# Kernel optimization log

Hardware: AMD Instinct MI355X
Metric: run time of the kernel (lower is better)

Reference implementation:

```python
import jax, jax.numpy as jnp
import numpy as np

N, F, H, C = 2048, 32, 64, 2
NEG = 0.01  # leaky_relu slope
BN_EPS = 1e-5


def _bn(h, g, b):
    m = h.mean(axis=0)
    v = h.var(axis=0)  # biased, as torch BN uses for normalization
    return (h - m) * jax.lax.rsqrt(v + BN_EPS) * g + b


def _gin(x, src, dst, eps, Wa, ba, Wb, bb):
    # PyG GINConv: out = mlp((1+eps)*x + sum_{j->i} x_j), messages flow src->dst
    agg = jax.ops.segment_sum(x[src], dst, num_segments=N)
    h = (1.0 + eps) * x + agg
    h = jax.nn.relu(h @ Wa + ba)
    return jax.nn.relu(h @ Wb + bb)


def setup_inputs() -> dict:
    key = jax.random.key(0)
    ks = jax.random.split(key, 16)
    src_np, dst_np = np.triu_indices(N, k=1)  # torch.combinations(arange(N), r=2)
    d = {
        'x': jnp.zeros((1,), jnp.float32),
        'node_features': jax.random.uniform(ks[0], (N, F), jnp.float32),
        'eps1': jnp.zeros((), jnp.float32),
        'W1a': jax.random.normal(ks[1], (F, H), jnp.float32) * 0.1,
        'b1a': jnp.zeros((H,), jnp.float32),
        'W1b': jax.random.normal(ks[2], (H, H), jnp.float32) * 0.1,
        'b1b': jnp.zeros((H,), jnp.float32),
        'epsm': jnp.zeros((), jnp.float32),
        'Wma': jax.random.normal(ks[3], (H, H), jnp.float32) * 0.1,
        'bma': jnp.zeros((H,), jnp.float32),
        'Wmb': jax.random.normal(ks[4], (H, H), jnp.float32) * 0.1,
        'bmb': jnp.zeros((H,), jnp.float32),
        'bnm_g': jnp.ones((H,), jnp.float32),
        'bnm_b': jnp.zeros((H,), jnp.float32),
        'epsl': jnp.zeros((), jnp.float32),
        'Wla': jax.random.normal(ks[5], (H, H), jnp.float32) * 0.1,
        'bla': jnp.zeros((H,), jnp.float32),
        'Wlb': jax.random.normal(ks[6], (H, F), jnp.float32) * 0.1,
        'blb': jnp.zeros((F,), jnp.float32),
        'W5': jax.random.normal(ks[7], (F, H), jnp.float32) * 0.1,
        'b5': jnp.zeros((H,), jnp.float32),
        'bn5_g': jnp.ones((H,), jnp.float32),
        'bn5_b': jnp.zeros((H,), jnp.float32),
        'W6': jax.random.normal(ks[8], (H, C), jnp.float32) * 0.1,
        'b6': jnp.zeros((C,), jnp.float32),
        'edge_src': jnp.asarray(src_np, jnp.int32),
        'edge_dst': jnp.asarray(dst_np, jnp.int32),
    }
    return d


def reference(x, node_features, eps1, W1a, b1a, W1b, b1b,
              epsm, Wma, bma, Wmb, bmb, bnm_g, bnm_b,
              epsl, Wla, bla, Wlb, blb,
              W5, b5, bn5_g, bn5_b, W6, b6,
              edge_src, edge_dst):
    xinit = node_features
    h = node_features
    # conv1 + leaky_relu
    h = jax.nn.leaky_relu(_gin(h, edge_src, edge_dst, eps1, W1a, b1a, W1b, b1b), NEG)
    # middle conv + leaky_relu + BN
    h = _gin(h, edge_src, edge_dst, epsm, Wma, bma, Wmb, bmb)
    h = jax.nn.leaky_relu(h, NEG)
    h = _bn(h, bnm_g, bnm_b)
    # last conv (back to F channels)
    h = _gin(h, edge_src, edge_dst, epsl, Wla, bla, Wlb, blb)
    h = h + xinit
    # edge predictor: gather-mul-MLP
    x_i = h[edge_src]
    x_j = h[edge_dst]
    e = jax.nn.leaky_relu((x_i * x_j) @ W5 + b5, NEG)
    e = _bn(e, bn5_g, bn5_b)
    logits = e @ W6 + b6
    p = jax.nn.softmax(logits, axis=-1)  # [E, C]
    # scatter into symmetric dense NxNxC tensor
    probs = jnp.zeros((N, N, C), jnp.float32)
    probs = probs.at[edge_src, edge_dst].set(p)
    probs = probs.at[edge_dst, edge_src].set(p)
    return probs
```

## Files before the change

kernel.cpp:

```cpp
#include <hip/hip_runtime.h>
#include <math.h>

#define NN 2048

typedef __attribute__((ext_vector_type(8))) short short8;
typedef __attribute__((ext_vector_type(4))) float f32x4;

__device__ inline short f2bf(float x) {
  union { float f; unsigned u; } v; v.f = x;
  unsigned r = v.u + 0x7fff + ((v.u >> 16) & 1);
  return (short)(r >> 16);
}
__device__ inline float bf2f(short h) {
  union { unsigned u; float f; } t;
  t.u = ((unsigned)(unsigned short)h) << 16;
  return t.f;
}

__global__ __launch_bounds__(256) void k_init(
    const float* __restrict__ nf, const float* __restrict__ W5,
    float* __restrict__ cs1, short* __restrict__ w5hi, short* __restrict__ w5lo,
    double* __restrict__ zbase) {
  __shared__ float sm[256];
  int tid = threadIdx.x, blk = blockIdx.x;
  int gtid = blk * 256 + tid;
  int node0 = blk * 32;
  if (gtid < 10240) zbase[gtid] = 0.0;
  if (gtid < 2048) {
    int c = gtid >> 5, k = gtid & 31;
    float wv = W5[k * 64 + c];
    short hi = f2bf(wv);
    w5hi[c * 32 + k] = hi;
    w5lo[c * 32 + k] = f2bf(wv - bf2f(hi));
  }
  int f = tid & 31, g = tid >> 5;
  float acc = 0.f;
#pragma unroll
  for (int k = 0; k < 4; k++) acc += nf[(size_t)(node0 + g * 4 + k) * 32 + f];
  sm[g * 32 + f] = acc;
  __syncthreads();
  if (tid < 32) {
    float s = 0.f;
#pragma unroll
    for (int g2 = 0; g2 < 8; g2++) s += sm[g2 * 32 + tid];
    cs1[blk * 32 + tid] = s;
  }
}

template <int FIN, int FOUT, bool STATS, bool ADDX, bool AFFINE, bool CSUM>
__global__ __launch_bounds__(256) void k_mlp32(
    const float* __restrict__ X, const float* __restrict__ CS,
    const float* __restrict__ epsp,
    const float* __restrict__ Wa, const float* __restrict__ ba,
    const float* __restrict__ Wb, const float* __restrict__ bb,
    float* __restrict__ OUT, const float* __restrict__ XINIT,
    double* __restrict__ statsW, const double* __restrict__ statsRd,
    const float* __restrict__ bng, const float* __restrict__ bnb,
    float* __restrict__ csum) {
  __shared__ float xh[32 * (FIN + 1)];
  __shared__ float Ts[32 * 65];
  __shared__ float Was[FIN * 64];
  __shared__ float Wbs[64 * FOUT];
  __shared__ float spref[FIN];
  __shared__ float part[4 * FIN];
  __shared__ float bas[64];
  __shared__ float bbs[FOUT];
  __shared__ float ssum[64];
  __shared__ float ssq[64];
  __shared__ float affa[64];
  __shared__ float affb[64];
  int tid = threadIdx.x;
  int blk = blockIdx.x;
  int node0 = blk * 32;
  float ep = 1.f + epsp[0];

  if (AFFINE) {
    if (tid < 64) {
      double s1 = 0.0, s2 = 0.0;
#pragma unroll
      for (int r = 0; r < 16; r++) {
        s1 += statsRd[r * 128 + tid];
        s2 += statsRd[r * 128 + 64 + tid];
      }
      double mean = s1 * (1.0 / 2048.0);
      double var = s2 * (1.0 / 2048.0) - mean * mean;
      if (var < 0.0) var = 0.0;
      float a = (float)((double)bng[tid] / sqrt(var + 1e-5));
      affa[tid] = a;
      affb[tid] = fmaf(-(float)mean, a, bnb[tid]);
    }
    __syncthreads();
  }

  for (int idx = tid; idx < 32 * FIN / 4; idx += 256) {
    int row = idx / (FIN / 4), c4 = (idx % (FIN / 4)) * 4;
    float4 v = *(const float4*)(X + (size_t)(node0 + row) * FIN + c4);
    if (AFFINE) {
      v.x = fmaf(affa[c4 + 0], v.x, affb[c4 + 0]);
      v.y = fmaf(affa[c4 + 1], v.y, affb[c4 + 1]);
      v.z = fmaf(affa[c4 + 2], v.z, affb[c4 + 2]);
      v.w = fmaf(affa[c4 + 3], v.w, affb[c4 + 3]);
    }
    float* dst = xh + row * (FIN + 1) + c4;
    dst[0] = v.x; dst[1] = v.y; dst[2] = v.z; dst[3] = v.w;
  }
  if (tid < 4 * FIN) {
    int g = tid / FIN, f = tid % FIN;
    float s = 0.f;
    for (int c = g; c < blk; c += 4) s += CS[c * FIN + f];
    part[tid] = s;
  }
  for (int idx = tid; idx < FIN * 16; idx += 256)
    *(float4*)(Was + idx * 4) = *(const float4*)(Wa + idx * 4);
  for (int idx = tid; idx < FOUT * 16; idx += 256)
    *(float4*)(Wbs + idx * 4) = *(const float4*)(Wb + idx * 4);
  if (tid < 64) bas[tid] = ba[tid];
  if (tid < FOUT) bbs[tid] = bb[tid];
  if ((STATS || CSUM) && tid < 64) { ssum[tid] = 0.f; ssq[tid] = 0.f; }
  __syncthreads();

  if (tid < FIN) {
    float s = part[tid] + part[FIN + tid] + part[2 * FIN + tid] + part[3 * FIN + tid];
    if (AFFINE) s = fmaf(affa[tid], s, (float)(32 * blk) * affb[tid]);
    spref[tid] = s;
  }
  __syncthreads();

  {
    int w = tid >> 6, lane = tid & 63, half = lane >> 5, nl = lane & 31;
#pragma unroll
    for (int p = 0; p < FIN / 8; p++) {
      int f = w * (FIN / 4) + 2 * p + half;
      float v = xh[nl * (FIN + 1) + f];
      float s = v;
#pragma unroll
      for (int d = 1; d < 32; d <<= 1) {
        float t = __shfl_up(s, (unsigned)d, 32);
        if (nl >= d) s += t;
      }
      xh[nl * (FIN + 1) + f] = fmaf(ep, v, spref[f] + (s - v));
    }
  }
  __syncthreads();

  {
    int n = tid >> 3, c0 = (tid & 7) * 8;
    float acc[8];
#pragma unroll
    for (int k = 0; k < 8; k++) acc[k] = bas[c0 + k];
    for (int f = 0; f < FIN; f++) {
      float xv = xh[n * (FIN + 1) + f];
#pragma unroll
      for (int k = 0; k < 8; k++) acc[k] = fmaf(xv, Was[f * 64 + c0 + k], acc[k]);
    }
#pragma unroll
    for (int k = 0; k < 8; k++) Ts[n * 65 + c0 + k] = fmaxf(acc[k], 0.f);
  }
  __syncthreads();

  {
    constexpr int CC = FOUT / 8;
    int n = tid >> 3, c0 = (tid & 7) * CC;
    float acc[CC];
#pragma unroll
    for (int k = 0; k < CC; k++) acc[k] = bbs[c0 + k];
    for (int f = 0; f < 64; f++) {
      float tv = Ts[n * 65 + f];
#pragma unroll
      for (int k = 0; k < CC; k++) acc[k] = fmaf(tv, Wbs[f * FOUT + c0 + k], acc[k]);
    }
#pragma unroll
    for (int k = 0; k < CC; k++) {
      float r = fmaxf(acc[k], 0.f);
      if (STATS || CSUM) atomicAdd(&ssum[c0 + k], r);
      if (STATS) atomicAdd(&ssq[c0 + k], r * r);
      if (ADDX) r += XINIT[(size_t)(node0 + n) * FOUT + c0 + k];
      OUT[(size_t)(node0 + n) * FOUT + c0 + k] = r;
    }
  }
  if (STATS || CSUM) {
    __syncthreads();
    if (tid < FOUT) {
      if (CSUM) csum[blk * FOUT + tid] = ssum[tid];
      if (STATS) {
        int rep = blk & 15;
        atomicAdd(&statsW[rep * 128 + tid], (double)ssum[tid]);
        atomicAdd(&statsW[rep * 128 + 64 + tid], (double)ssq[tid]);
      }
    }
  }
}

__device__ inline void tile_decode(int t, int& bi, int& bj) {
  bi = (int)((257.0f - sqrtf(66049.0f - 8.0f * (float)t)) * 0.5f);
  if (bi > 127) bi = 127;
  while (bi > 0 && bi * (257 - bi) / 2 > t) bi--;
  while ((bi + 1) * (256 - bi) / 2 <= t) bi++;
  bj = bi + (t - bi * (257 - bi) / 2);
}

__device__ inline void split_pack(const float m[8], short8& ah, short8& al) {
  unsigned uh[8], ul[8];
#pragma unroll
  for (int e = 0; e < 8; e++) {
    union { float f; unsigned u; } um; um.f = m[e];
    uh[e] = um.u;
    union { unsigned u; float f; } hf; hf.u = um.u & 0xffff0000u;
    union { float f; unsigned u; } lf; lf.f = m[e] - hf.f;
    ul[e] = lf.u;
  }
  union { unsigned i[4]; short8 s; } ph, pl;
#pragma unroll
  for (int k = 0; k < 4; k++) {
    ph.i[k] = __builtin_amdgcn_perm(uh[2 * k + 1], uh[2 * k], 0x07060302u);
    pl.i[k] = __builtin_amdgcn_perm(ul[2 * k + 1], ul[2 * k], 0x07060302u);
  }
  ah = ph.s;
  al = pl.s;
}

__device__ inline f32x4 mfma3b(short8 ah, short8 al, short8 bh, short8 bl, float bias) {
  f32x4 z = (f32x4){bias, bias, bias, bias};
  z = __builtin_amdgcn_mfma_f32_16x16x32_bf16(al, bh, z, 0, 0, 0);
  z = __builtin_amdgcn_mfma_f32_16x16x32_bf16(ah, bl, z, 0, 0, 0);
  z = __builtin_amdgcn_mfma_f32_16x16x32_bf16(ah, bh, z, 0, 0, 0);
  return z;
}

__global__ __launch_bounds__(256) void k_edge1m(
    const float* __restrict__ H3, const short* __restrict__ W5Th,
    const short* __restrict__ W5Tl, const float* __restrict__ b5,
    double* __restrict__ stats5, int T, int stride) {
  __shared__ float sI[16][36];
  __shared__ float sJ[16][36];
  __shared__ float ssum[64], ssq[64];
  int tid = threadIdx.x;
  int w = tid >> 6, lane = tid & 63;
  int quad = lane >> 4, l15 = lane & 15;
  int q8 = quad * 8;
  if (tid < 64) { ssum[tid] = 0.f; ssq[tid] = 0.f; }

  short8 bh[4], bl[4];
  float b5v[4];
#pragma unroll
  for (int nt = 0; nt < 4; nt++) {
    bh[nt] = *(const short8*)(W5Th + (nt * 16 + l15) * 32 + q8);
    bl[nt] = *(const short8*)(W5Tl + (nt * 16 + l15) * 32 + q8);
    b5v[nt] = b5[nt * 16 + l15];
  }
  float accS[4] = {0.f, 0.f, 0.f, 0.f}, accQ[4] = {0.f, 0.f, 0.f, 0.f};

  for (int t = blockIdx.x; t < T; t += stride) {
    int bi, bj;
    tile_decode(t, bi, bj);
    __syncthreads();
    {
      int row = tid >> 3, c4 = (tid & 7) * 4;
      int grow = (row < 16) ? (bi * 16 + row) : (bj * 16 + row - 16);
      float4 v = *(const float4*)(H3 + (size_t)grow * 32 + c4);
      float* dst = (row < 16) ? &sI[row][c4] : &sJ[row - 16][c4];
      *(float4*)dst = v;
    }
    __syncthreads();
    const float* pJ = &sJ[l15][q8];
    float4 j0 = *(const float4*)pJ, j1 = *(const float4*)(pJ + 4);
    short8 ah[4], al[4];
#pragma unroll
    for (int mt = 0; mt < 4; mt++) {
      const float* pI = &sI[4 * w + mt][q8];
      float4 i0 = *(const float4*)pI, i1 = *(const float4*)(pI + 4);
      float m[8] = {i0.x * j0.x, i0.y * j0.y, i0.z * j0.z, i0.w * j0.w,
                    i1.x * j1.x, i1.y * j1.y, i1.z * j1.z, i1.w * j1.w};
      split_pack(m, ah[mt], al[mt]);
    }
    bool diag = (bi == bj);
#pragma unroll
    for (int mt = 0; mt < 4; mt++) {
      int iRow = bi * 16 + 4 * w + mt;
#pragma unroll
      for (int nt = 0; nt < 4; nt++) {
        f32x4 z = mfma3b(ah[mt], al[mt], bh[nt], bl[nt], b5v[nt]);
#pragma unroll
        for (int r = 0; r < 4; r++) {
          float e = fmaxf(z[r], z[r] * 0.01f);
          if (diag) {
            int jCol = bj * 16 + quad * 4 + r;
            e = (iRow < jCol) ? e : 0.f;
          }
          accS[nt] += e;
          accQ[nt] = fmaf(e, e, accQ[nt]);
        }
      }
    }
  }
#pragma unroll
  for (int nt = 0; nt < 4; nt++) {
    accS[nt] += __shfl_xor(accS[nt], 16); accS[nt] += __shfl_xor(accS[nt], 32);
    accQ[nt] += __shfl_xor(accQ[nt], 16); accQ[nt] += __shfl_xor(accQ[nt], 32);
  }
  if (quad == 0) {
#pragma unroll
    for (int nt = 0; nt < 4; nt++) {
      atomicAdd(&ssum[nt * 16 + l15], accS[nt]);
      atomicAdd(&ssq[nt * 16 + l15], accQ[nt]);
    }
  }
  __syncthreads();
  if (tid < 64) {
    int rep = blockIdx.x & 63;
    atomicAdd(&stats5[rep * 128 + tid], (double)ssum[tid]);
    atomicAdd(&stats5[rep * 128 + 64 + tid], (double)ssq[tid]);
  }
}

__global__ void k_prep5(const double* __restrict__ stats5, const float* __restrict__ g,
                        const float* __restrict__ bb, const float* __restrict__ W6,
                        const float* __restrict__ b6, float* __restrict__ prep,
                        double ecnt) {
  __shared__ float s0s[64], s1s[64];
  int c = threadIdx.x;
  if (c < 64) {
    double s1 = 0.0, s2 = 0.0;
    for (int r = 0; r < 64; r++) {
      s1 += stats5[r * 128 + c];
      s2 += stats5[r * 128 + 64 + c];
    }
    double mean = s1 / ecnt;
    double var = s2 / ecnt - mean * mean;
    if (var < 0.0) var = 0.0;
    float a = (float)((double)g[c] / sqrt(var + 1e-5));
    float sh = (float)((double)bb[c] - mean * (double)a);
    float w6a = W6[2 * c], w6b = W6[2 * c + 1];
    prep[c] = a * w6a;
    prep[64 + c] = a * w6b;
    s0s[c] = sh * w6a;
    s1s[c] = sh * w6b;
  }
  __syncthreads();
  if (c == 0) { float t = b6[0]; for (int k = 0; k < 64; k++) t += s0s[k]; prep[128] = t; }
  if (c == 1) { float t = b6[1]; for (int k = 0; k < 64; k++) t += s1s[k]; prep[129] = t; }
}

__global__ __launch_bounds__(256) void k_edge2m(
    const float* __restrict__ H3, const short* __restrict__ W5Th,
    const short* __restrict__ W5Tl, const float* __restrict__ b5,
    const float* __restrict__ prep, float* __restrict__ outp, int T, int stride) {
  __shared__ float sI[16][36];
  __shared__ float sJ[16][36];
  int tid = threadIdx.x;
  int w = tid >> 6, lane = tid & 63;
  int quad = lane >> 4, l15 = lane & 15;
  int q8 = quad * 8;

  short8 bh[4], bl[4];
  float b5v[4], sw0v[4], sw1v[4];
#pragma unroll
  for (int nt = 0; nt < 4; nt++) {
    int c = nt * 16 + l15;
    bh[nt] = *(const short8*)(W5Th + c * 32 + q8);
    bl[nt] = *(const short8*)(W5Tl + c * 32 + q8);
    b5v[nt] = b5[c];
    sw0v[nt] = prep[c];
    sw1v[nt] = prep[64 + c];
  }
  float base0 = prep[128], base1 = prep[129];

  for (int t = blockIdx.x; t < T; t += stride) {
    int bi, bj;
    tile_decode(t, bi, bj);
    __syncthreads();
    {
      int row = tid >> 3, c4 = (tid & 7) * 4;
      int grow = (row < 16) ? (bi * 16 + row) : (bj * 16 + row - 16);
      float4 v = *(const float4*)(H3 + (size_t)grow * 32 + c4);
      float* dst = (row < 16) ? &sI[row][c4] : &sJ[row - 16][c4];
      *(float4*)dst = v;
    }
    __syncthreads();
    const float* pJ = &sJ[l15][q8];
    float4 j0 = *(const float4*)pJ, j1 = *(const float4*)(pJ + 4);
    short8 ah[4], al[4];
#pragma unroll
    for (int mt = 0; mt < 4; mt++) {
      const float* pI = &sI[4 * w + mt][q8];
      float4 i0 = *(const float4*)pI, i1 = *(const float4*)(pI + 4);
      float m[8] = {i0.x * j0.x, i0.y * j0.y, i0.z * j0.z, i0.w * j0.w,
                    i1.x * j1.x, i1.y * j1.y, i1.z * j1.z, i1.w * j1.w};
      split_pack(m, ah[mt], al[mt]);
    }
    float c0a[16], c1a[16];
#pragma unroll
    for (int mt = 0; mt < 4; mt++) {
#pragma unroll
      for (int nt = 0; nt < 4; nt++) {
        f32x4 z = mfma3b(ah[mt], al[mt], bh[nt], bl[nt], b5v[nt]);
#pragma unroll
        for (int r = 0; r < 4; r++) {
          float e = fmaxf(z[r], z[r] * 0.01f);
          if (nt == 0) {
            c0a[mt * 4 + r] = e * sw0v[0];
            c1a[mt * 4 + r] = e * sw1v[0];
          } else {
            c0a[mt * 4 + r] = fmaf(e, sw0v[nt], c0a[mt * 4 + r]);
            c1a[mt * 4 + r] = fmaf(e, sw1v[nt], c1a[mt * 4 + r]);
          }
        }
      }
    }
    float n0[8], n1[8];
    {
      int up = l15 & 8;
#pragma unroll
      for (int k = 0; k < 8; k++) {
        float s0 = up ? c0a[k] : c0a[8 + k];
        float s1 = up ? c1a[k] : c1a[8 + k];
        n0[k] = (up ? c0a[8 + k] : c0a[k]) + __shfl_xor(s0, 8);
        n1[k] = (up ? c1a[8 + k] : c1a[k]) + __shfl_xor(s1, 8);
      }
    }
    float q0[4], q1[4];
    {
      int up = l15 & 4;
#pragma unroll
      for (int k = 0; k < 4; k++) {
        float s0 = up ? n0[k] : n0[4 + k];
        float s1 = up ? n1[k] : n1[4 + k];
        q0[k] = (up ? n0[4 + k] : n0[k]) + __shfl_xor(s0, 4);
        q1[k] = (up ? n1[4 + k] : n1[k]) + __shfl_xor(s1, 4);
      }
    }
    float d0[2], d1[2];
    {
      int up = l15 & 2;
#pragma unroll
      for (int k = 0; k < 2; k++) {
        float s0 = up ? q0[k] : q0[2 + k];
        float s1 = up ? q1[k] : q1[2 + k];
        d0[k] = (up ? q0[2 + k] : q0[k]) + __shfl_xor(s0, 2);
        d1[k] = (up ? q1[2 + k] : q1[k]) + __shfl_xor(s1, 2);
      }
    }
    float f0, f1;
    {
      int up = l15 & 1;
      float s0 = up ? d0[0] : d0[1];
      float s1 = up ? d1[0] : d1[1];
      f0 = (up ? d0[1] : d0[0]) + __shfl_xor(s0, 1);
      f1 = (up ? d1[1] : d1[0]) + __shfl_xor(s1, 1);
    }
    int i = bi * 16 + 4 * w + (l15 >> 2);
    int j = bj * 16 + quad * 4 + (l15 & 3);
    if (i < j) {
      float dlt = (f1 + base1) - (f0 + base0);
      float ex = __expf(dlt);
      float p0 = 1.f / (1.f + ex);
      float2 p = make_float2(p0, ex * p0);
      *(float2*)(outp + ((size_t)i * NN + j) * 2) = p;
      *(float2*)(outp + ((size_t)j * NN + i) * 2) = p;
    } else if (i == j) {
      *(float2*)(outp + ((size_t)i * NN + i) * 2) = make_float2(0.f, 0.f);
    }
  }
}

extern "C" void kernel_launch(void* const* d_in, const int* in_sizes, int n_in,
                              void* d_out, int out_size, void* d_ws, size_t ws_size,
                              hipStream_t stream) {
  const float* nf   = (const float*)d_in[1];
  const float* eps1 = (const float*)d_in[2];
  const float* W1a  = (const float*)d_in[3];
  const float* b1a  = (const float*)d_in[4];
  const float* W1b  = (const float*)d_in[5];
  const float* b1b  = (const float*)d_in[6];
  const float* epsm = (const float*)d_in[7];
  const float* Wma  = (const float*)d_in[8];
  const float* bma  = (const float*)d_in[9];
  const float* Wmb  = (const float*)d_in[10];
  const float* bmb  = (const float*)d_in[11];
  const float* bnmg = (const float*)d_in[12];
  const float* bnmb = (const float*)d_in[13];
  const float* epsl = (const float*)d_in[14];
  const float* Wla  = (const float*)d_in[15];
  const float* bla  = (const float*)d_in[16];
  const float* Wlb  = (const float*)d_in[17];
  const float* blb  = (const float*)d_in[18];
  const float* W5   = (const float*)d_in[19];
  const float* b5   = (const float*)d_in[20];
  const float* bn5g = (const float*)d_in[21];
  const float* bn5b = (const float*)d_in[22];
  const float* W6   = (const float*)d_in[23];
  const float* b6   = (const float*)d_in[24];
  double ecnt = (double)in_sizes[25];
  float* out = (float*)d_out;

  float* w = (float*)d_ws;
  float* h1   = w;
  float* h2   = w + 131072;
  float* h3   = w + 262144;
  float* cs1  = w + 327680;
  float* cs2  = w + 329728;
  float* csr  = w + 333824;
  float* prep = w + 337920;
  short* w5hi = (short*)(w + 338112);
  short* w5lo = (short*)(w + 339136);
  double* statsM = (double*)(w + 340160);
  double* stats5 = statsM + 2048;

  k_init<<<64, 256, 0, stream>>>(nf, W5, cs1, w5hi, w5lo, statsM);
  k_mlp32<32, 64, false, false, false, true><<<64, 256, 0, stream>>>(
      nf, cs1, eps1, W1a, b1a, W1b, b1b, h1, nullptr, nullptr, nullptr,
      nullptr, nullptr, cs2);
  k_mlp32<64, 64, true, false, false, true><<<64, 256, 0, stream>>>(
      h1, cs2, epsm, Wma, bma, Wmb, bmb, h2, nullptr, statsM, nullptr,
      nullptr, nullptr, csr);
  k_mlp32<64, 32, false, true, true, false><<<64, 256, 0, stream>>>(
      h2, csr, epsl, Wla, bla, Wlb, blb, h3, nf, nullptr, statsM,
      bnmg, bnmb, nullptr);

  const int T = 8256;
  const int NB = 2064;
  k_edge1m<<<NB, 256, 0, stream>>>(h3, w5hi, w5lo, b5, stats5, T, NB);
  k_prep5<<<1, 64, 0, stream>>>(stats5, bn5g, bn5b, W6, b6, prep, ecnt);
  k_edge2m<<<NB, 256, 0, stream>>>(h3, w5hi, w5lo, b5, prep, out, T, NB);
}
```

Before: 277.3 us.

## Fold 2-class softmax into logit difference and swap MFMA operands in edge2m

Folds the two-class softmax into a single logit difference, so prep holds one weight vector plus one base term and the second-pass edge kernel computes one dot product per edge instead of two. The MFMA operands are swapped so the W5 fragments act as the A operand and the edge products as B. The 64-channel reduction then becomes per-lane accumulation plus two cross-quad shuffles, replacing the four-stage butterfly. The persistent grid-stride loop is replaced by one block per tile, which drops the per-iteration syncthreads but re-loads the weights in every block.

```diff
diff --git a/kernel.cpp b/kernel.cpp
--- a/kernel.cpp
+++ b/kernel.cpp
@@ -317,7 +317,7 @@
                         const float* __restrict__ bb, const float* __restrict__ W6,
                         const float* __restrict__ b6, float* __restrict__ prep,
                         double ecnt) {
-  __shared__ float s0s[64], s1s[64];
+  __shared__ float sdel[64];
   int c = threadIdx.x;
   if (c < 64) {
     double s1 = 0.0, s2 = 0.0;
@@ -330,136 +330,88 @@
     if (var < 0.0) var = 0.0;
     float a = (float)((double)g[c] / sqrt(var + 1e-5));
     float sh = (float)((double)bb[c] - mean * (double)a);
-    float w6a = W6[2 * c], w6b = W6[2 * c + 1];
-    prep[c] = a * w6a;
-    prep[64 + c] = a * w6b;
-    s0s[c] = sh * w6a;
-    s1s[c] = sh * w6b;
-  }
-  __syncthreads();
-  if (c == 0) { float t = b6[0]; for (int k = 0; k < 64; k++) t += s0s[k]; prep[128] = t; }
-  if (c == 1) { float t = b6[1]; for (int k = 0; k < 64; k++) t += s1s[k]; prep[129] = t; }
+    float dw = W6[2 * c + 1] - W6[2 * c];
+    prep[c] = a * dw;
+    sdel[c] = sh * dw;
+  }
+  __syncthreads();
+  if (c == 0) {
+    float t = b6[1] - b6[0];
+    for (int k = 0; k < 64; k++) t += sdel[k];
+    prep[64] = t;
+  }
 }
 
 __global__ __launch_bounds__(256) void k_edge2m(
     const float* __restrict__ H3, const short* __restrict__ W5Th,
     const short* __restrict__ W5Tl, const float* __restrict__ b5,
-    const float* __restrict__ prep, float* __restrict__ outp, int T, int stride) {
+    const float* __restrict__ prep, float* __restrict__ outp) {
   __shared__ float sI[16][36];
   __shared__ float sJ[16][36];
   int tid = threadIdx.x;
   int w = tid >> 6, lane = tid & 63;
   int quad = lane >> 4, l15 = lane & 15;
   int q8 = quad * 8;
-
-  short8 bh[4], bl[4];
-  float b5v[4], sw0v[4], sw1v[4];
+  int bi, bj;
+  tile_decode(blockIdx.x, bi, bj);
+  {
+    int row = tid >> 3, c4 = (tid & 7) * 4;
+    int grow = (row < 16) ? (bi * 16 + row) : (bj * 16 + row - 16);
+    float4 v = *(const float4*)(H3 + (size_t)grow * 32 + c4);
+    float* dst = (row < 16) ? &sI[row][c4] : &sJ[row - 16][c4];
+    *(float4*)dst = v;
+  }
+  short8 ah[4], al[4];
+  f32x4 b5v[4], uv[4];
+#pragma unroll
+  for (int Mt = 0; Mt < 4; Mt++) {
+    ah[Mt] = *(const short8*)(W5Th + (Mt * 16 + l15) * 32 + q8);
+    al[Mt] = *(const short8*)(W5Tl + (Mt * 16 + l15) * 32 + q8);
+    b5v[Mt] = *(const f32x4*)(b5 + Mt * 16 + quad * 4);
+    uv[Mt] = *(const f32x4*)(prep + Mt * 16 + quad * 4);
+  }
+  float dbase = prep[64];
+  __syncthreads();
+
+  const float* pJ = &sJ[l15][q8];
+  float4 j0 = *(const float4*)pJ, j1 = *(const float4*)(pJ + 4);
+  float dkeep = 0.f;
 #pragma unroll
   for (int nt = 0; nt < 4; nt++) {
-    int c = nt * 16 + l15;
-    bh[nt] = *(const short8*)(W5Th + c * 32 + q8);
-    bl[nt] = *(const short8*)(W5Tl + c * 32 + q8);
-    b5v[nt] = b5[c];
-    sw0v[nt] = prep[c];
-    sw1v[nt] = prep[64 + c];
-  }
-  float base0 = prep[128], base1 = prep[129];
-
-  for (int t = blockIdx.x; t < T; t += stride) {
-    int bi, bj;
-    tile_decode(t, bi, bj);
-    __syncthreads();
-    {
-      int row = tid >> 3, c4 = (tid & 7) * 4;
-      int grow = (row < 16) ? (bi * 16 + row) : (bj * 16 + row - 16);
-      float4 v = *(const float4*)(H3 + (size_t)grow * 32 + c4);
-      float* dst = (row < 16) ? &sI[row][c4] : &sJ[row - 16][c4];
-      *(float4*)dst = v;
-    }
-    __syncthreads();
-    const float* pJ = &sJ[l15][q8];
-    float4 j0 = *(const float4*)pJ, j1 = *(const float4*)(pJ + 4);
-    short8 ah[4], al[4];
-#pragma unroll
-    for (int mt = 0; mt < 4; mt++) {
-      const float* pI = &sI[4 * w + mt][q8];
-      float4 i0 = *(const float4*)pI, i1 = *(const float4*)(pI + 4);
-      float m[8] = {i0.x * j0.x, i0.y * j0.y, i0.z * j0.z, i0.w * j0.w,
-                    i1.x * j1.x, i1.y * j1.y, i1.z * j1.z, i1.w * j1.w};
-      split_pack(m, ah[mt], al[mt]);
-    }
-    float c0a[16], c1a[16];
-#pragma unroll
-    for (int mt = 0; mt < 4; mt++) {
-#pragma unroll
-      for (int nt = 0; nt < 4; nt++) {
-        f32x4 z = mfma3b(ah[mt], al[mt], bh[nt], bl[nt], b5v[nt]);
-#pragma unroll
-        for (int r = 0; r < 4; r++) {
-          float e = fmaxf(z[r], z[r] * 0.01f);
-          if (nt == 0) {
-            c0a[mt * 4 + r] = e * sw0v[0];
-            c1a[mt * 4 + r] = e * sw1v[0];
-          } else {
-            c0a[mt * 4 + r] = fmaf(e, sw0v[nt], c0a[mt * 4 + r]);
-            c1a[mt * 4 + r] = fmaf(e, sw1v[nt], c1a[mt * 4 + r]);
-          }
-        }
+    const float* pI = &sI[4 * w + nt][q8];
+    float4 i0 = *(const float4*)pI, i1 = *(const float4*)(pI + 4);
+    float m[8] = {i0.x * j0.x, i0.y * j0.y, i0.z * j0.z, i0.w * j0.w,
+                  i1.x * j1.x, i1.y * j1.y, i1.z * j1.z, i1.w * j1.w};
+    short8 bh, bl;
+    split_pack(m, bh, bl);
+    float d = 0.f;
+#pragma unroll
+    for (int Mt = 0; Mt < 4; Mt++) {
+      f32x4 z = b5v[Mt];
+      z = __builtin_amdgcn_mfma_f32_16x16x32_bf16(al[Mt], bh, z, 0, 0, 0);
+      z = __builtin_amdgcn_mfma_f32_16x16x32_bf16(ah[Mt], bl, z, 0, 0, 0);
+      z = __builtin_amdgcn_mfma_f32_16x16x32_bf16(ah[Mt], bh, z, 0, 0, 0);
+#pragma unroll
+      for (int r = 0; r < 4; r++) {
+        float e = fmaxf(z[r], z[r] * 0.01f);
+        d = fmaf(e, uv[Mt][r], d);
       }
     }
-    float n0[8], n1[8];
-    {
-      int up = l15 & 8;
-#pragma unroll
-      for (int k = 0; k < 8; k++) {
-        float s0 = up ? c0a[k] : c0a[8 + k];
-        float s1 = up ? c1a[k] : c1a[8 + k];
-        n0[k] = (up ? c0a[8 + k] : c0a[k]) + __shfl_xor(s0, 8);
-        n1[k] = (up ? c1a[8 + k] : c1a[k]) + __shfl_xor(s1, 8);
-      }
-    }
-    float q0[4], q1[4];
-    {
-      int up = l15 & 4;
-#pragma unroll
-      for (int k = 0; k < 4; k++) {
-        float s0 = up ? n0[k] : n0[4 + k];
-        float s1 = up ? n1[k] : n1[4 + k];
-        q0[k] = (up ? n0[4 + k] : n0[k]) + __shfl_xor(s0, 4);
-        q1[k] = (up ? n1[4 + k] : n1[k]) + __shfl_xor(s1, 4);
-      }
-    }
-    float d0[2], d1[2];
-    {
-      int up = l15 & 2;
-#pragma unroll
-      for (int k = 0; k < 2; k++) {
-        float s0 = up ? q0[k] : q0[2 + k];
-        float s1 = up ? q1[k] : q1[2 + k];
-        d0[k] = (up ? q0[2 + k] : q0[k]) + __shfl_xor(s0, 2);
-        d1[k] = (up ? q1[2 + k] : q1[k]) + __shfl_xor(s1, 2);
-      }
-    }
-    float f0, f1;
-    {
-      int up = l15 & 1;
-      float s0 = up ? d0[0] : d0[1];
-      float s1 = up ? d1[0] : d1[1];
-      f0 = (up ? d0[1] : d0[0]) + __shfl_xor(s0, 1);
-      f1 = (up ? d1[1] : d1[0]) + __shfl_xor(s1, 1);
-    }
-    int i = bi * 16 + 4 * w + (l15 >> 2);
-    int j = bj * 16 + quad * 4 + (l15 & 3);
-    if (i < j) {
-      float dlt = (f1 + base1) - (f0 + base0);
-      float ex = __expf(dlt);
-      float p0 = 1.f / (1.f + ex);
-      float2 p = make_float2(p0, ex * p0);
-      *(float2*)(outp + ((size_t)i * NN + j) * 2) = p;
-      *(float2*)(outp + ((size_t)j * NN + i) * 2) = p;
-    } else if (i == j) {
-      *(float2*)(outp + ((size_t)i * NN + i) * 2) = make_float2(0.f, 0.f);
-    }
+    d += __shfl_xor(d, 16);
+    d += __shfl_xor(d, 32);
+    if (quad == nt) dkeep = d;
+  }
+  int i = bi * 16 + 4 * w + quad;
+  int j = bj * 16 + l15;
+  if (i < j) {
+    float dd = dkeep + dbase;
+    float ex = __expf(dd);
+    float p0 = 1.f / (1.f + ex);
+    float2 p = make_float2(p0, ex * p0);
+    *(float2*)(outp + ((size_t)i * NN + j) * 2) = p;
+    *(float2*)(outp + ((size_t)j * NN + i) * 2) = p;
+  } else if (i == j) {
+    *(float2*)(outp + ((size_t)i * NN + i) * 2) = make_float2(0.f, 0.f);
   }
 }
 
@@ -521,5 +473,5 @@
   const int NB = 2064;
   k_edge1m<<<NB, 256, 0, stream>>>(h3, w5hi, w5lo, b5, stats5, T, NB);
   k_prep5<<<1, 64, 0, stream>>>(stats5, bn5g, bn5b, W6, b6, prep, ecnt);
-  k_edge2m<<<NB, 256, 0, stream>>>(h3, w5hi, w5lo, b5, prep, out, T, NB);
-}
+  k_edge2m<<<T, 256, 0, stream>>>(h3, w5hi, w5lo, b5, prep, out);
+}
```

Result: faster. 255.3 us (-7.9%).
